# Performance work log

Measured on AMD Instinct MI355X. Metric: run time of the kernel, lower is better.

The kernel has to match this reference:

```python
import jax, jax.numpy as jnp
import numpy as np

N, E, H, IN, C, L, G = 50000, 600000, 128, 128, 4, 3, 128
EPS = 1e-5
BN_SCALE = 1.0 / np.sqrt(1.0 + EPS)  # eval BN with running_mean=0, running_var=1


def _bn(x, g, b):
    return x * (g * BN_SCALE) + b


def _gelu(x):
    return jax.nn.gelu(x, approximate=False)


def setup_inputs() -> dict:
    key = jax.random.key(0)
    ks = jax.random.split(key, 40)
    s = 0.02
    d = {}
    d['x'] = jax.random.normal(ks[0], (N, IN), jnp.float32)
    d['edge_index'] = jax.random.randint(ks[1], (2, E), 0, N)
    d['batch'] = jnp.sort(jax.random.randint(ks[2], (N,), 0, G))
    # input projection
    d['W1'] = jax.random.normal(ks[3], (IN, H)) * s; d['b1'] = jnp.zeros((H,))
    d['g1'] = jnp.ones((H,)); d['be1'] = jnp.zeros((H,))
    d['W2'] = jax.random.normal(ks[4], (H, H)) * s; d['b2'] = jnp.zeros((H,))
    d['g2'] = jnp.ones((H,)); d['be2'] = jnp.zeros((H,))
    # GCN layers (stacked over L)
    d['Wg'] = jax.random.normal(ks[5], (L, H, H)) * s
    d['bg'] = jnp.zeros((L, H))
    d['gg'] = jnp.ones((L, H)); d['bgg'] = jnp.zeros((L, H))
    # graph attention weights
    d['Wa1'] = jax.random.normal(ks[6], (H, H // 2)) * s; d['ba1'] = jnp.zeros((H // 2,))
    d['Wa2'] = jax.random.normal(ks[7], (H // 2, 1)) * s; d['ba2'] = jnp.zeros((1,))
    # classifier
    d['Wc1'] = jax.random.normal(ks[8], (4 * H, 2 * H)) * s; d['bc1'] = jnp.zeros((2 * H,))
    d['gc1'] = jnp.ones((2 * H,)); d['bec1'] = jnp.zeros((2 * H,))
    d['Wc2'] = jax.random.normal(ks[9], (2 * H, H)) * s; d['bc2'] = jnp.zeros((H,))
    d['gc2'] = jnp.ones((H,)); d['bec2'] = jnp.zeros((H,))
    d['Wc3'] = jax.random.normal(ks[10], (H, H // 2)) * s; d['bc3'] = jnp.zeros((H // 2,))
    d['gc3'] = jnp.ones((H // 2,)); d['bec3'] = jnp.zeros((H // 2,))
    d['Wc4'] = jax.random.normal(ks[11], (H // 2, C)) * s; d['bc4'] = jnp.zeros((C,))
    return d


def reference(x, edge_index, batch, W1, b1, g1, be1, W2, b2, g2, be2,
              Wg, bg, gg, bgg, Wa1, ba1, Wa2, ba2,
              Wc1, bc1, gc1, bec1, Wc2, bc2, gc2, bec2,
              Wc3, bc3, gc3, bec3, Wc4, bc4):
    n = x.shape[0]
    src, dst = edge_index[0], edge_index[1]
    # input projection (dropout off in eval)
    h = _gelu(_bn(x @ W1 + b1, g1, be1))
    h = _gelu(_bn(h @ W2 + b2, g2, be2))
    # GCN symmetric norm with self-loops (PyG GCNConv semantics)
    deg = jax.ops.segment_sum(jnp.ones_like(src, dtype=h.dtype), dst, n) + 1.0
    dinv = jax.lax.rsqrt(deg)
    enorm = (dinv[src] * dinv[dst])[:, None]   # [E,1]
    snorm = (dinv * dinv)[:, None]             # [N,1] self-loop weight
    for i in range(L):
        xw = h @ Wg[i]
        agg = jax.ops.segment_sum(xw[src] * enorm, dst, n) + xw * snorm
        h = _gelu(_bn(agg + bg[i], gg[i], bgg[i])) + h
    # attention weights per node
    aw = jnp.tanh(_gelu(h @ Wa1 + ba1) @ Wa2 + ba2)  # [N,1]
    # multi-branch pooling per graph
    cnt = jnp.maximum(jax.ops.segment_sum(jnp.ones((n,), h.dtype), batch, G), 1.0)[:, None]
    x_mean = jax.ops.segment_sum(h, batch, G) / cnt
    x_max = jax.ops.segment_max(h, batch, G)
    x_weighted = jax.ops.segment_sum(h * aw, batch, G) / cnt
    comb = jnp.concatenate([x_mean, x_max, x_mean, x_weighted], axis=-1)  # x_transformer_pooled == x_mean
    z = _gelu(_bn(comb @ Wc1 + bc1, gc1, bec1))
    z = _gelu(_bn(z @ Wc2 + bc2, gc2, bec2))
    z = _gelu(_bn(z @ Wc3 + bc3, gc3, bec3))
    return z @ Wc4 + bc4
```

## Files before the change

kernel.cpp:

```cpp
#include <hip/hip_runtime.h>
#include <hip/hip_bf16.h>
#include <float.h>


#define GGRAPHS 128
#define POOL_NC 16

typedef __attribute__((ext_vector_type(8))) short short8b;
typedef __attribute__((ext_vector_type(4))) float f32x4;

__device__ __forceinline__ float gelu_f(float x) {
    return 0.5f * x * (1.0f + erff(x * 0.7071067811865476f));
}

__device__ __forceinline__ unsigned short f2bf(float f) {
    unsigned int u = __float_as_uint(f);
    unsigned int r = (u + 0x7FFFu + ((u >> 16) & 1u)) >> 16;
    return (unsigned short)r;
}

__device__ __forceinline__ float bf2f(unsigned short u) {
    return __uint_as_float(((unsigned int)u) << 16);
}

static constexpr float BNS_F = 0.99999500003749968f;

__global__ void transpose_all_kernel(const float* __restrict__ W1, const float* __restrict__ W2,
                                     const float* __restrict__ Wg, const float* __restrict__ Wa1,
                                     unsigned short* __restrict__ Wt1, unsigned short* __restrict__ Wt2,
                                     unsigned short* __restrict__ Wtg, unsigned short* __restrict__ Wta1)
{
    const int id = blockIdx.x * 256 + threadIdx.x;
    if (id < 81920) {
        const int m = id >> 14;
        const int r = id & 16383;
        const int k = r >> 7, c = r & 127;
        const float* Wsrc = (m == 0) ? W1 : (m == 1) ? W2 : Wg + (size_t)(m - 2) * 16384;
        unsigned short* Wdst = (m == 0) ? Wt1 : (m == 1) ? Wt2 : Wtg + (size_t)(m - 2) * 16384;
        Wdst[c * 128 + k] = f2bf(Wsrc[r]);
    } else if (id < 90112) {
        const int r = id - 81920;
        const int k = r >> 6, c = r & 63;
        Wta1[c * 128 + k] = f2bf(Wa1[r]);
    }
}

template<int M, bool A_FP32, bool DO_BN, bool DO_GELU, bool DO_RES, bool DO_AW>
__global__ __launch_bounds__(256, 2)
void gemm_mfma(const void* __restrict__ Ain,
               const unsigned short* __restrict__ Wtb,
               const float* __restrict__ bias, const float* __restrict__ gam,
               const float* __restrict__ beta, const unsigned short* __restrict__ residb,
               unsigned short* __restrict__ Ybf,
               const float* __restrict__ Wa2, const float* __restrict__ ba2,
               float* __restrict__ awout, int nrows)
{
    constexpr int NCT = M / 16;
    __shared__ unsigned short Wl[M * 128];

    const int tid = threadIdx.x;

    constexpr int NCH = M * 16;
#pragma unroll
    for (int i = 0; i < NCH / 256; ++i) {
        const int idx = i * 256 + tid;
        const uint4 v = reinterpret_cast<const uint4*>(Wtb)[idx];
        const int byte = idx * 16;
        const int swz = byte ^ (((byte >> 8) & 7) << 4);
        *reinterpret_cast<uint4*>(reinterpret_cast<char*>(Wl) + swz) = v;
    }
    __syncthreads();

    const int w = tid >> 6;
    const int l = tid & 63;
    const int l4 = l >> 4, lm = l & 15;
    const int rowbase = (int)blockIdx.x * 64 + w * 16;

    int arow = rowbase + lm; if (arow >= nrows) arow = nrows - 1;
    short8b a[4];
    if constexpr (A_FP32) {
        const float* apf = (const float*)Ain + (size_t)arow * 128 + l4 * 8;
#pragma unroll
        for (int ks = 0; ks < 4; ++ks) {
            const float4 v0 = *reinterpret_cast<const float4*>(apf + ks * 32);
            const float4 v1 = *reinterpret_cast<const float4*>(apf + ks * 32 + 4);
            short8b av;
            av[0] = (short)f2bf(v0.x); av[1] = (short)f2bf(v0.y);
            av[2] = (short)f2bf(v0.z); av[3] = (short)f2bf(v0.w);
            av[4] = (short)f2bf(v1.x); av[5] = (short)f2bf(v1.y);
            av[6] = (short)f2bf(v1.z); av[7] = (short)f2bf(v1.w);
            a[ks] = av;
        }
    } else {
        const unsigned short* ap = (const unsigned short*)Ain + (size_t)arow * 128 + l4 * 8;
#pragma unroll
        for (int ks = 0; ks < 4; ++ks)
            a[ks] = *reinterpret_cast<const short8b*>(ap + ks * 32);
    }

    f32x4 acc[NCT];
#pragma unroll
    for (int ct = 0; ct < NCT; ++ct) acc[ct] = f32x4{0.f, 0.f, 0.f, 0.f};

    const int swzm = (lm & 7) << 4;
    const char* Wlc = reinterpret_cast<const char*>(Wl);
#pragma unroll
    for (int ks = 0; ks < 4; ++ks) {
#pragma unroll
        for (int ct = 0; ct < NCT; ++ct) {
            const int byte = ct * 4096 + lm * 256 + ks * 64 + l4 * 16;
            const short8b bv = *reinterpret_cast<const short8b*>(Wlc + (byte ^ swzm));
            acc[ct] = __builtin_amdgcn_mfma_f32_16x16x32_bf16(a[ks], bv, acc[ct], 0, 0, 0);
        }
    }

    if (DO_AW) {
        float p[4] = {0.f, 0.f, 0.f, 0.f};
#pragma unroll
        for (int ct = 0; ct < NCT; ++ct) {
            const int col = ct * 16 + lm;
            float sc, bi;
            if (DO_BN) { float g = gam[col]; sc = g * BNS_F; bi = bias[col] * sc + beta[col]; }
            else       { sc = 1.f; bi = bias[col]; }
            const float wa = Wa2[col];
#pragma unroll
            for (int rid = 0; rid < 4; ++rid) {
                float v = acc[ct][rid] * sc + bi;
                if (DO_GELU) v = gelu_f(v);
                p[rid] = fmaf(v, wa, p[rid]);
            }
        }
        const float ba2v = ba2[0];
#pragma unroll
        for (int rid = 0; rid < 4; ++rid) {
            float v = p[rid];
            v += __shfl_xor(v, 1);
            v += __shfl_xor(v, 2);
            v += __shfl_xor(v, 4);
            v += __shfl_xor(v, 8);
            const int row = rowbase + l4 * 4 + rid;
            if (lm == 0 && row < nrows) awout[row] = tanhf(v + ba2v);
        }
        return;
    }

#pragma unroll
    for (int ct = 0; ct < NCT; ++ct) {
        const int col = ct * 16 + lm;
        float sc, bi;
        if (DO_BN) { float g = gam[col]; sc = g * BNS_F; bi = bias[col] * sc + beta[col]; }
        else       { sc = 1.f; bi = bias[col]; }
#pragma unroll
        for (int rid = 0; rid < 4; ++rid) {
            const int row = rowbase + l4 * 4 + rid;
            if (row < nrows) {
                float v = acc[ct][rid] * sc + bi;
                if (DO_GELU) v = gelu_f(v);
                if (DO_RES) v += bf2f(residb[(size_t)row * M + col]);
                Ybf[(size_t)row * M + col] = f2bf(v);
            }
        }
    }
}

__global__ void count_rank_kernel(const int* __restrict__ dst, int* __restrict__ cnt,
                                  int* __restrict__ rank, int E)
{
    int e = blockIdx.x * 256 + threadIdx.x;
    if (e < E) rank[e] = atomicAdd(&cnt[dst[e]], 1);
}

__global__ void scan_local(const int* __restrict__ cnt, int* __restrict__ rowptr,
                           int* __restrict__ bsum, float* __restrict__ dinv, int n)
{
    __shared__ int sd[1024];
    const int tid = threadIdx.x;
    const int i = blockIdx.x * 1024 + tid;
    int v = (i < n) ? cnt[i] : 0;
    if (i < n) dinv[i] = rsqrtf((float)v + 1.0f);
    sd[tid] = v;
    __syncthreads();
    for (int off = 1; off < 1024; off <<= 1) {
        int t = (tid >= off) ? sd[tid - off] : 0;
        __syncthreads();
        sd[tid] += t;
        __syncthreads();
    }
    if (i < n) rowptr[i + 1] = sd[tid];
    if (tid == 1023) bsum[blockIdx.x] = sd[1023];
}

__global__ void scan_bsum(int* __restrict__ bsum, int nb)
{
    const int lane = threadIdx.x;
    int orig = (lane < nb) ? bsum[lane] : 0;
    int v = orig;
#pragma unroll
    for (int off = 1; off < 64; off <<= 1) {
        int t = __shfl_up(v, off);
        if (lane >= off) v += t;
    }
    if (lane < nb) bsum[lane] = v - orig;
}

__global__ void scan_add(int* __restrict__ rowptr, const int* __restrict__ bsum, int n)
{
    const int i = blockIdx.x * 1024 + threadIdx.x;
    if (i < n) rowptr[i + 1] += bsum[blockIdx.x];
    if (i == 0) rowptr[0] = 0;
}

__global__ void fill_kernel(const int* __restrict__ src, const int* __restrict__ dst,
                            const float* __restrict__ dinv, const int* __restrict__ rowptr,
                            const int* __restrict__ rank, int2* __restrict__ csr, int E)
{
    int e = blockIdx.x * 256 + threadIdx.x;
    if (e < E) {
        const int d = dst[e], s = src[e];
        const int pos = rowptr[d] + rank[e];
        int2 p;
        p.x = s;
        p.y = __float_as_int(dinv[s] * dinv[d]);
        csr[pos] = p;
    }
}

#define FMAB(A, Wt, U) { A.x = fmaf(Wt, bf2f(U.x), A.x); A.y = fmaf(Wt, bf2f(U.y), A.y); \
                         A.z = fmaf(Wt, bf2f(U.z), A.z); A.w = fmaf(Wt, bf2f(U.w), A.w); }

__global__ __launch_bounds__(256)
void agg_kernel(const ushort4* __restrict__ hb, const int2* __restrict__ csr,
                const int* __restrict__ rowptr, const float* __restrict__ dinv,
                ushort4* __restrict__ ahb, int n)
{
    const int node = blockIdx.x * 8 + (threadIdx.x >> 5);
    if (node >= n) return;
    const int lane = threadIdx.x & 31;

    const float di = dinv[node];
    const float sw = di * di;
    const ushort4 sv = hb[(size_t)node * 32 + lane];
    float4 a0, a1;
    a0.x = bf2f(sv.x) * sw; a0.y = bf2f(sv.y) * sw;
    a0.z = bf2f(sv.z) * sw; a0.w = bf2f(sv.w) * sw;
    a1.x = 0.f; a1.y = 0.f; a1.z = 0.f; a1.w = 0.f;

    const int beg = rowptr[node], end = rowptr[node + 1];
    int s = beg;
    for (; s + 4 <= end; s += 4) {
        const int2 e0 = csr[s+0], e1 = csr[s+1], e2 = csr[s+2], e3 = csr[s+3];
        const ushort4 v0 = hb[(size_t)e0.x * 32 + lane];
        const ushort4 v1 = hb[(size_t)e1.x * 32 + lane];
        const ushort4 v2 = hb[(size_t)e2.x * 32 + lane];
        const ushort4 v3 = hb[(size_t)e3.x * 32 + lane];
        FMAB(a0, __int_as_float(e0.y), v0); FMAB(a1, __int_as_float(e1.y), v1);
        FMAB(a0, __int_as_float(e2.y), v2); FMAB(a1, __int_as_float(e3.y), v3);
    }
    for (; s < end; ++s) {
        const int2 e0 = csr[s];
        const ushort4 v = hb[(size_t)e0.x * 32 + lane];
        FMAB(a0, __int_as_float(e0.y), v);
    }
    ushort4 q;
    q.x = f2bf(a0.x + a1.x); q.y = f2bf(a0.y + a1.y);
    q.z = f2bf(a0.z + a1.z); q.w = f2bf(a0.w + a1.w);
    ahb[(size_t)node * 32 + lane] = q;
}

__device__ __forceinline__ int lb_batch(const int* __restrict__ batch, int n, int t)
{
    int lo = 0, hi = n;
    while (lo < hi) { int mid = (lo + hi) >> 1; if (batch[mid] < t) lo = mid + 1; else hi = mid; }
    return lo;
}

__global__ void pool_partial(const unsigned short* __restrict__ h, const float* __restrict__ aw,
                             const int* __restrict__ batch, int n, float* __restrict__ ps,
                             float* __restrict__ pm, float* __restrict__ pw)
{
    const int g = blockIdx.x >> 4;
    const int c = blockIdx.x & (POOL_NC - 1);
    const int f = threadIdx.x;
    const int beg = lb_batch(batch, n, g), end = lb_batch(batch, n, g + 1);
    const int len = end - beg;
    const int cbeg = beg + (int)(((long long)len * c) / POOL_NC);
    const int cend = beg + (int)(((long long)len * (c + 1)) / POOL_NC);
    float s = 0.f, m = -FLT_MAX, w = 0.f;
    for (int node = cbeg; node < cend; ++node) {
        const float v = bf2f(h[(size_t)node * 128 + f]);
        const float a = aw[node];
        s += v;
        m = fmaxf(m, v);
        w = fmaf(v, a, w);
    }
    const size_t idx = ((size_t)g * POOL_NC + c) * 128 + f;
    ps[idx] = s; pm[idx] = m; pw[idx] = w;
}

__global__ void pool_final(const float* __restrict__ ps, const float* __restrict__ pm,
                           const float* __restrict__ pw, const int* __restrict__ batch,
                           int n, float* __restrict__ comb)
{
    const int g = blockIdx.x;
    const int f = threadIdx.x;
    float s = 0.f, m = -FLT_MAX, w = 0.f;
#pragma unroll
    for (int c = 0; c < POOL_NC; ++c) {
        const size_t idx = ((size_t)g * POOL_NC + c) * 128 + f;
        s += ps[idx];
        m = fmaxf(m, pm[idx]);
        w += pw[idx];
    }
    float cn = (float)(lb_batch(batch, n, g + 1) - lb_batch(batch, n, g));
    if (cn < 1.f) cn = 1.f;
    comb[(size_t)g * 512 + f]       = s / cn;
    comb[(size_t)g * 512 + 128 + f] = m;
    comb[(size_t)g * 512 + 256 + f] = s / cn;
    comb[(size_t)g * 512 + 384 + f] = w / cn;
}

template<int K, int M, bool DO_BN, bool DO_GELU>
__global__ __launch_bounds__(256)
void rowgemm2(const float* __restrict__ X, const float* __restrict__ W,
              const float* __restrict__ bias, const float* __restrict__ gam,
              const float* __restrict__ beta, float* __restrict__ Y)
{
    constexpr int NC = M / 64;
    constexpr int KQ = K / 4;
    const int row = blockIdx.x / NC;
    const int lane = threadIdx.x & 63;
    const int c = (blockIdx.x % NC) * 64 + lane;
    const int q = threadIdx.x >> 6;

    const float* __restrict__ xq = X + (size_t)row * K + q * KQ;
    const float* __restrict__ wq = W + (size_t)(q * KQ) * M + c;

    float a0 = 0.f, a1 = 0.f, a2 = 0.f, a3 = 0.f;
#pragma unroll 4
    for (int k = 0; k < KQ; k += 4) {
        const float4 xv = *reinterpret_cast<const float4*>(xq + k);
        a0 = fmaf(xv.x, wq[(size_t)(k + 0) * M], a0);
        a1 = fmaf(xv.y, wq[(size_t)(k + 1) * M], a1);
        a2 = fmaf(xv.z, wq[(size_t)(k + 2) * M], a2);
        a3 = fmaf(xv.w, wq[(size_t)(k + 3) * M], a3);
    }
    __shared__ float part[4][64];
    part[q][lane] = (a0 + a1) + (a2 + a3);
    __syncthreads();
    if (q == 0) {
        float v = (part[0][lane] + part[1][lane]) + (part[2][lane] + part[3][lane]);
        if (DO_BN) { const float g = gam[c]; const float sc = g * BNS_F; v = v * sc + (bias[c] * sc + beta[c]); }
        else       { v = v + bias[c]; }
        if (DO_GELU) v = gelu_f(v);
        Y[(size_t)row * M + c] = v;
    }
}

__global__ void rowgemm_final(const float* __restrict__ X, const float* __restrict__ W,
                              const float* __restrict__ bias, float* __restrict__ Y)
{
    const int row = blockIdx.x;
    const int lane = threadIdx.x;
    const float xv = X[(size_t)row * 64 + lane];
    const float4 wr = *reinterpret_cast<const float4*>(W + lane * 4);
    float a0 = xv * wr.x, a1 = xv * wr.y, a2 = xv * wr.z, a3 = xv * wr.w;
#pragma unroll
    for (int off = 32; off; off >>= 1) {
        a0 += __shfl_xor(a0, off);
        a1 += __shfl_xor(a1, off);
        a2 += __shfl_xor(a2, off);
        a3 += __shfl_xor(a3, off);
    }
    if (lane == 0) {
        Y[(size_t)row * 4 + 0] = a0 + bias[0];
        Y[(size_t)row * 4 + 1] = a1 + bias[1];
        Y[(size_t)row * 4 + 2] = a2 + bias[2];
        Y[(size_t)row * 4 + 3] = a3 + bias[3];
    }
}

extern "C" void kernel_launch(void* const* d_in, const int* in_sizes, int n_in,
                              void* d_out, int out_size, void* d_ws, size_t ws_size,
                              hipStream_t stream)
{
    const float* x     = (const float*)d_in[0];
    const int*   ei    = (const int*)d_in[1];
    const int*   batch = (const int*)d_in[2];
    const float* W1  = (const float*)d_in[3];
    const float* b1  = (const float*)d_in[4];
    const float* g1  = (const float*)d_in[5];
    const float* be1 = (const float*)d_in[6];
    const float* W2  = (const float*)d_in[7];
    const float* b2  = (const float*)d_in[8];
    const float* g2  = (const float*)d_in[9];
    const float* be2 = (const float*)d_in[10];
    const float* Wg  = (const float*)d_in[11];
    const float* bg  = (const float*)d_in[12];
    const float* gg  = (const float*)d_in[13];
    const float* bgg = (const float*)d_in[14];
    const float* Wa1 = (const float*)d_in[15];
    const float* ba1 = (const float*)d_in[16];
    const float* Wa2 = (const float*)d_in[17];
    const float* ba2 = (const float*)d_in[18];
    const float* Wc1 = (const float*)d_in[19];
    const float* bc1 = (const float*)d_in[20];
    const float* gc1 = (const float*)d_in[21];
    const float* bec1= (const float*)d_in[22];
    const float* Wc2 = (const float*)d_in[23];
    const float* bc2 = (const float*)d_in[24];
    const float* gc2 = (const float*)d_in[25];
    const float* bec2= (const float*)d_in[26];
    const float* Wc3 = (const float*)d_in[27];
    const float* bc3 = (const float*)d_in[28];
    const float* gc3 = (const float*)d_in[29];
    const float* bec3= (const float*)d_in[30];
    const float* Wc4 = (const float*)d_in[31];
    const float* bc4 = (const float*)d_in[32];
    float* out = (float*)d_out;

    const int N = in_sizes[0] / 128;
    const int E = in_sizes[1] / 2;
    const int G = GGRAPHS;

    size_t off = 0;
    auto alloc = [&](size_t bytes) -> void* {
        void* p = (char*)d_ws + off;
        off += (bytes + 255) & ~(size_t)255;
        return p;
    };
    unsigned short* hAb   = (unsigned short*)alloc((size_t)N * 128 * 2);
    unsigned short* hbf   = (unsigned short*)alloc((size_t)N * 128 * 2);
    unsigned short* ahb   = (unsigned short*)alloc((size_t)N * 128 * 2);
    unsigned short* Wt1   = (unsigned short*)alloc(128 * 128 * 2);
    unsigned short* Wt2   = (unsigned short*)alloc(128 * 128 * 2);
    unsigned short* Wtg   = (unsigned short*)alloc(3 * 128 * 128 * 2);
    unsigned short* Wta1  = (unsigned short*)alloc(64 * 128 * 2);
    float*   aw     = (float*)alloc((size_t)N * 4);
    float*   dinv   = (float*)alloc((size_t)N * 4);
    int*     cnt    = (int*)alloc((size_t)N * 4);
    int*     rank   = (int*)alloc((size_t)E * 4);
    int*     rowptr = (int*)alloc((size_t)(N + 1) * 4);
    int*     bsum   = (int*)alloc(64 * 4);
    int2*    csr    = (int2*)alloc((size_t)E * 8);
    float*   comb   = (float*)alloc((size_t)G * 512 * 4);
    float*   ps     = (float*)alloc((size_t)G * POOL_NC * 128 * 4);
    float*   pm     = (float*)alloc((size_t)G * POOL_NC * 128 * 4);
    float*   pw     = (float*)alloc((size_t)G * POOL_NC * 128 * 4);
    float*   z1     = (float*)alloc((size_t)G * 256 * 4);
    float*   z2     = (float*)alloc((size_t)G * 128 * 4);
    float*   z3     = (float*)alloc((size_t)G * 64 * 4);
    (void)ws_size;

    const int* e_src = ei;
    const int* e_dst = ei + E;

    transpose_all_kernel<<<352, 256, 0, stream>>>(W1, W2, Wg, Wa1, Wt1, Wt2, Wtg, Wta1);

    hipMemsetAsync(cnt, 0, (size_t)N * 4, stream);
    count_rank_kernel<<<(E + 255) / 256, 256, 0, stream>>>(e_dst, cnt, rank, E);
    const int nb = (N + 1023) / 1024;
    scan_local<<<nb, 1024, 0, stream>>>(cnt, rowptr, bsum, dinv, N);
    scan_bsum<<<1, 64, 0, stream>>>(bsum, nb);
    scan_add<<<nb, 1024, 0, stream>>>(rowptr, bsum, N);
    fill_kernel<<<(E + 255) / 256, 256, 0, stream>>>(e_src, e_dst, dinv, rowptr, rank, csr, E);

    const int rowblocks = (N + 63) / 64;

    gemm_mfma<128, true, true, true, false, false><<<rowblocks, 256, 0, stream>>>(
        x, Wt1, b1, g1, be1, nullptr, hAb, nullptr, nullptr, nullptr, N);
    gemm_mfma<128, false, true, true, false, false><<<rowblocks, 256, 0, stream>>>(
        hAb, Wt2, b2, g2, be2, nullptr, hbf, nullptr, nullptr, nullptr, N);

    for (int l = 0; l < 3; ++l) {
        agg_kernel<<<(N + 7) / 8, 256, 0, stream>>>(
            (const ushort4*)hbf, csr, rowptr, dinv, (ushort4*)ahb, N);
        gemm_mfma<128, false, true, true, true, false><<<rowblocks, 256, 0, stream>>>(
            ahb, Wtg + (size_t)l * 16384, bg + (size_t)l * 128,
            gg + (size_t)l * 128, bgg + (size_t)l * 128, hbf, hbf,
            nullptr, nullptr, nullptr, N);
    }

    gemm_mfma<64, false, false, true, false, true><<<rowblocks, 256, 0, stream>>>(
        hbf, Wta1, ba1, nullptr, nullptr, nullptr, nullptr, Wa2, ba2, aw, N);

    pool_partial<<<G * POOL_NC, 128, 0, stream>>>(hbf, aw, batch, N, ps, pm, pw);
    pool_final<<<G, 128, 0, stream>>>(ps, pm, pw, batch, N, comb);

    rowgemm2<512, 256, true, true><<<G * 4, 256, 0, stream>>>(comb, Wc1, bc1, gc1, bec1, z1);
    rowgemm2<256, 128, true, true><<<G * 2, 256, 0, stream>>>(z1, Wc2, bc2, gc2, bec2, z2);
    rowgemm2<128, 64,  true, true><<<G * 1, 256, 0, stream>>>(z2, Wc3, bc3, gc3, bec3, z3);
    rowgemm_final<<<G, 64, 0, stream>>>(z3, Wc4, bc4, out);
}
```

Baseline: 382.6 us.

## Fuse input projection GEMMs and last GCN GEMM with attention GEMM via LDS

Merges the two input-projection GEMMs into one kernel that keeps the intermediate activation in swizzled LDS instead of writing and re-reading it from global memory. Fuses the final GCN layer GEMM with the attention-weight GEMM, reusing the freshly computed h tile from LDS. Also folds the single-block bsum scan into scan_add, so one launch is removed. The fused kernels use more LDS per block (up to 80KB), which may lower occupancy.

```diff
diff --git a/kernel.cpp b/kernel.cpp
--- a/kernel.cpp
+++ b/kernel.cpp
@@ -45,63 +45,24 @@
     }
 }
 
-template<int M, bool A_FP32, bool DO_BN, bool DO_GELU, bool DO_RES, bool DO_AW>
-__global__ __launch_bounds__(256, 2)
-void gemm_mfma(const void* __restrict__ Ain,
-               const unsigned short* __restrict__ Wtb,
-               const float* __restrict__ bias, const float* __restrict__ gam,
-               const float* __restrict__ beta, const unsigned short* __restrict__ residb,
-               unsigned short* __restrict__ Ybf,
-               const float* __restrict__ Wa2, const float* __restrict__ ba2,
-               float* __restrict__ awout, int nrows)
-{
-    constexpr int NCT = M / 16;
-    __shared__ unsigned short Wl[M * 128];
-
-    const int tid = threadIdx.x;
-
-    constexpr int NCH = M * 16;
-#pragma unroll
-    for (int i = 0; i < NCH / 256; ++i) {
+template<int M>
+__device__ __forceinline__ void stage_wt(const unsigned short* __restrict__ Wtb,
+                                         unsigned short* __restrict__ Wl, int tid)
+{
+#pragma unroll
+    for (int i = 0; i < (M * 16) / 256; ++i) {
         const int idx = i * 256 + tid;
         const uint4 v = reinterpret_cast<const uint4*>(Wtb)[idx];
         const int byte = idx * 16;
         const int swz = byte ^ (((byte >> 8) & 7) << 4);
         *reinterpret_cast<uint4*>(reinterpret_cast<char*>(Wl) + swz) = v;
     }
-    __syncthreads();
-
-    const int w = tid >> 6;
-    const int l = tid & 63;
-    const int l4 = l >> 4, lm = l & 15;
-    const int rowbase = (int)blockIdx.x * 64 + w * 16;
-
-    int arow = rowbase + lm; if (arow >= nrows) arow = nrows - 1;
-    short8b a[4];
-    if constexpr (A_FP32) {
-        const float* apf = (const float*)Ain + (size_t)arow * 128 + l4 * 8;
-#pragma unroll
-        for (int ks = 0; ks < 4; ++ks) {
-            const float4 v0 = *reinterpret_cast<const float4*>(apf + ks * 32);
-            const float4 v1 = *reinterpret_cast<const float4*>(apf + ks * 32 + 4);
-            short8b av;
-            av[0] = (short)f2bf(v0.x); av[1] = (short)f2bf(v0.y);
-            av[2] = (short)f2bf(v0.z); av[3] = (short)f2bf(v0.w);
-            av[4] = (short)f2bf(v1.x); av[5] = (short)f2bf(v1.y);
-            av[6] = (short)f2bf(v1.z); av[7] = (short)f2bf(v1.w);
-            a[ks] = av;
-        }
-    } else {
-        const unsigned short* ap = (const unsigned short*)Ain + (size_t)arow * 128 + l4 * 8;
-#pragma unroll
-        for (int ks = 0; ks < 4; ++ks)
-            a[ks] = *reinterpret_cast<const short8b*>(ap + ks * 32);
-    }
-
-    f32x4 acc[NCT];
-#pragma unroll
-    for (int ct = 0; ct < NCT; ++ct) acc[ct] = f32x4{0.f, 0.f, 0.f, 0.f};
-
+}
+
+template<int NCT>
+__device__ __forceinline__ void mfma_stage(const short8b* a, const unsigned short* __restrict__ Wl,
+                                           f32x4* acc, int l4, int lm)
+{
     const int swzm = (lm & 7) << 4;
     const char* Wlc = reinterpret_cast<const char*>(Wl);
 #pragma unroll
@@ -113,53 +74,246 @@
             acc[ct] = __builtin_amdgcn_mfma_f32_16x16x32_bf16(a[ks], bv, acc[ct], 0, 0, 0);
         }
     }
-
-    if (DO_AW) {
-        float p[4] = {0.f, 0.f, 0.f, 0.f};
-#pragma unroll
-        for (int ct = 0; ct < NCT; ++ct) {
-            const int col = ct * 16 + lm;
-            float sc, bi;
-            if (DO_BN) { float g = gam[col]; sc = g * BNS_F; bi = bias[col] * sc + beta[col]; }
-            else       { sc = 1.f; bi = bias[col]; }
-            const float wa = Wa2[col];
-#pragma unroll
-            for (int rid = 0; rid < 4; ++rid) {
-                float v = acc[ct][rid] * sc + bi;
-                if (DO_GELU) v = gelu_f(v);
-                p[rid] = fmaf(v, wa, p[rid]);
-            }
+}
+
+__device__ __forceinline__ void load_afrag_bf(const unsigned short* __restrict__ ap, short8b* a)
+{
+#pragma unroll
+    for (int ks = 0; ks < 4; ++ks)
+        a[ks] = *reinterpret_cast<const short8b*>(ap + ks * 32);
+}
+
+__device__ __forceinline__ void load_afrag_lds(const unsigned short* __restrict__ hl,
+                                               int rowl, int l4, short8b* a)
+{
+    const char* hc = reinterpret_cast<const char*>(hl);
+    const int swz = (rowl & 7) << 4;
+#pragma unroll
+    for (int ks = 0; ks < 4; ++ks) {
+        const int byte = rowl * 256 + ks * 64 + l4 * 16;
+        a[ks] = *reinterpret_cast<const short8b*>(hc + (byte ^ swz));
+    }
+}
+
+__device__ __forceinline__ void store_h_lds(unsigned short* __restrict__ hl,
+                                            int rowl, int col, unsigned short v)
+{
+    const int byte = (rowl * 256 + col * 2) ^ ((rowl & 7) << 4);
+    *reinterpret_cast<unsigned short*>(reinterpret_cast<char*>(hl) + byte) = v;
+}
+
+__global__ __launch_bounds__(256, 2)
+void proj_fused(const float* __restrict__ x,
+                const unsigned short* __restrict__ Wt1, const unsigned short* __restrict__ Wt2,
+                const float* __restrict__ b1, const float* __restrict__ g1, const float* __restrict__ be1,
+                const float* __restrict__ b2, const float* __restrict__ g2, const float* __restrict__ be2,
+                unsigned short* __restrict__ hbf, int nrows)
+{
+    __shared__ unsigned short W1l[128 * 128];
+    __shared__ unsigned short W2l[128 * 128];
+    __shared__ unsigned short h1l[64 * 128];
+
+    const int tid = threadIdx.x;
+    stage_wt<128>(Wt1, W1l, tid);
+    stage_wt<128>(Wt2, W2l, tid);
+    __syncthreads();
+
+    const int w = tid >> 6;
+    const int l = tid & 63;
+    const int l4 = l >> 4, lm = l & 15;
+    const int rowbase = (int)blockIdx.x * 64 + w * 16;
+
+    int arow = rowbase + lm; if (arow >= nrows) arow = nrows - 1;
+    const float* apf = x + (size_t)arow * 128 + l4 * 8;
+    short8b a[4];
+#pragma unroll
+    for (int ks = 0; ks < 4; ++ks) {
+        const float4 v0 = *reinterpret_cast<const float4*>(apf + ks * 32);
+        const float4 v1 = *reinterpret_cast<const float4*>(apf + ks * 32 + 4);
+        short8b av;
+        av[0] = (short)f2bf(v0.x); av[1] = (short)f2bf(v0.y);
+        av[2] = (short)f2bf(v0.z); av[3] = (short)f2bf(v0.w);
+        av[4] = (short)f2bf(v1.x); av[5] = (short)f2bf(v1.y);
+        av[6] = (short)f2bf(v1.z); av[7] = (short)f2bf(v1.w);
+        a[ks] = av;
+    }
+
+    f32x4 acc[8];
+#pragma unroll
+    for (int ct = 0; ct < 8; ++ct) acc[ct] = f32x4{0.f, 0.f, 0.f, 0.f};
+    mfma_stage<8>(a, W1l, acc, l4, lm);
+
+#pragma unroll
+    for (int ct = 0; ct < 8; ++ct) {
+        const int col = ct * 16 + lm;
+        const float g = g1[col];
+        const float sc = g * BNS_F;
+        const float bi = b1[col] * sc + be1[col];
+#pragma unroll
+        for (int rid = 0; rid < 4; ++rid) {
+            const int rowl = w * 16 + l4 * 4 + rid;
+            float v = acc[ct][rid] * sc + bi;
+            v = gelu_f(v);
+            store_h_lds(h1l, rowl, col, f2bf(v));
         }
-        const float ba2v = ba2[0];
-#pragma unroll
-        for (int rid = 0; rid < 4; ++rid) {
-            float v = p[rid];
-            v += __shfl_xor(v, 1);
-            v += __shfl_xor(v, 2);
-            v += __shfl_xor(v, 4);
-            v += __shfl_xor(v, 8);
-            const int row = rowbase + l4 * 4 + rid;
-            if (lm == 0 && row < nrows) awout[row] = tanhf(v + ba2v);
-        }
-        return;
-    }
-
-#pragma unroll
-    for (int ct = 0; ct < NCT; ++ct) {
+    }
+    __syncthreads();
+
+    load_afrag_lds(h1l, w * 16 + lm, l4, a);
+#pragma unroll
+    for (int ct = 0; ct < 8; ++ct) acc[ct] = f32x4{0.f, 0.f, 0.f, 0.f};
+    mfma_stage<8>(a, W2l, acc, l4, lm);
+
+#pragma unroll
+    for (int ct = 0; ct < 8; ++ct) {
         const int col = ct * 16 + lm;
-        float sc, bi;
-        if (DO_BN) { float g = gam[col]; sc = g * BNS_F; bi = bias[col] * sc + beta[col]; }
-        else       { sc = 1.f; bi = bias[col]; }
+        const float g = g2[col];
+        const float sc = g * BNS_F;
+        const float bi = b2[col] * sc + be2[col];
 #pragma unroll
         for (int rid = 0; rid < 4; ++rid) {
             const int row = rowbase + l4 * 4 + rid;
             if (row < nrows) {
                 float v = acc[ct][rid] * sc + bi;
-                if (DO_GELU) v = gelu_f(v);
-                if (DO_RES) v += bf2f(residb[(size_t)row * M + col]);
-                Ybf[(size_t)row * M + col] = f2bf(v);
+                v = gelu_f(v);
+                hbf[(size_t)row * 128 + col] = f2bf(v);
             }
         }
+    }
+}
+
+__global__ __launch_bounds__(256, 2)
+void gemm_gcn(const unsigned short* __restrict__ Abf,
+              const unsigned short* __restrict__ Wtb,
+              const float* __restrict__ bias, const float* __restrict__ gam,
+              const float* __restrict__ beta, unsigned short* __restrict__ hbf,
+              int nrows)
+{
+    __shared__ unsigned short Wl[128 * 128];
+
+    const int tid = threadIdx.x;
+    stage_wt<128>(Wtb, Wl, tid);
+    __syncthreads();
+
+    const int w = tid >> 6;
+    const int l = tid & 63;
+    const int l4 = l >> 4, lm = l & 15;
+    const int rowbase = (int)blockIdx.x * 64 + w * 16;
+
+    int arow = rowbase + lm; if (arow >= nrows) arow = nrows - 1;
+    short8b a[4];
+    load_afrag_bf(Abf + (size_t)arow * 128 + l4 * 8, a);
+
+    f32x4 acc[8];
+#pragma unroll
+    for (int ct = 0; ct < 8; ++ct) acc[ct] = f32x4{0.f, 0.f, 0.f, 0.f};
+    mfma_stage<8>(a, Wl, acc, l4, lm);
+
+#pragma unroll
+    for (int ct = 0; ct < 8; ++ct) {
+        const int col = ct * 16 + lm;
+        const float g = gam[col];
+        const float sc = g * BNS_F;
+        const float bi = bias[col] * sc + beta[col];
+#pragma unroll
+        for (int rid = 0; rid < 4; ++rid) {
+            const int row = rowbase + l4 * 4 + rid;
+            if (row < nrows) {
+                float v = acc[ct][rid] * sc + bi;
+                v = gelu_f(v);
+                v += bf2f(hbf[(size_t)row * 128 + col]);
+                hbf[(size_t)row * 128 + col] = f2bf(v);
+            }
+        }
+    }
+}
+
+__global__ __launch_bounds__(256, 2)
+void gcn_aw_fused(const unsigned short* __restrict__ Abf,
+                  const unsigned short* __restrict__ Wt3,
+                  const float* __restrict__ bias, const float* __restrict__ gam,
+                  const float* __restrict__ beta, unsigned short* __restrict__ hbf,
+                  const unsigned short* __restrict__ Wta1, const float* __restrict__ ba1,
+                  const float* __restrict__ Wa2, const float* __restrict__ ba2,
+                  float* __restrict__ awout, int nrows)
+{
+    __shared__ unsigned short W3l[128 * 128];
+    __shared__ unsigned short Wa1l[64 * 128];
+    __shared__ unsigned short hl[64 * 128];
+
+    const int tid = threadIdx.x;
+    stage_wt<128>(Wt3, W3l, tid);
+    stage_wt<64>(Wta1, Wa1l, tid);
+    __syncthreads();
+
+    const int w = tid >> 6;
+    const int l = tid & 63;
+    const int l4 = l >> 4, lm = l & 15;
+    const int rowbase = (int)blockIdx.x * 64 + w * 16;
+
+    int arow = rowbase + lm; if (arow >= nrows) arow = nrows - 1;
+    short8b a[4];
+    load_afrag_bf(Abf + (size_t)arow * 128 + l4 * 8, a);
+
+    f32x4 acc[8];
+#pragma unroll
+    for (int ct = 0; ct < 8; ++ct) acc[ct] = f32x4{0.f, 0.f, 0.f, 0.f};
+    mfma_stage<8>(a, W3l, acc, l4, lm);
+
+#pragma unroll
+    for (int ct = 0; ct < 8; ++ct) {
+        const int col = ct * 16 + lm;
+        const float g = gam[col];
+        const float sc = g * BNS_F;
+        const float bi = bias[col] * sc + beta[col];
+#pragma unroll
+        for (int rid = 0; rid < 4; ++rid) {
+            const int row = rowbase + l4 * 4 + rid;
+            const int rowl = w * 16 + l4 * 4 + rid;
+            float v = acc[ct][rid] * sc + bi;
+            v = gelu_f(v);
+            unsigned short hv;
+            if (row < nrows) {
+                v += bf2f(hbf[(size_t)row * 128 + col]);
+                hv = f2bf(v);
+                hbf[(size_t)row * 128 + col] = hv;
+            } else {
+                hv = 0;
+            }
+            store_h_lds(hl, rowl, col, hv);
+        }
+    }
+    __syncthreads();
+
+    load_afrag_lds(hl, w * 16 + lm, l4, a);
+    f32x4 acc2[4];
+#pragma unroll
+    for (int ct = 0; ct < 4; ++ct) acc2[ct] = f32x4{0.f, 0.f, 0.f, 0.f};
+    mfma_stage<4>(a, Wa1l, acc2, l4, lm);
+
+    float p[4] = {0.f, 0.f, 0.f, 0.f};
+#pragma unroll
+    for (int ct = 0; ct < 4; ++ct) {
+        const int col = ct * 16 + lm;
+        const float bi = ba1[col];
+        const float wa = Wa2[col];
+#pragma unroll
+        for (int rid = 0; rid < 4; ++rid) {
+            float v = acc2[ct][rid] + bi;
+            v = gelu_f(v);
+            p[rid] = fmaf(v, wa, p[rid]);
+        }
+    }
+    const float ba2v = ba2[0];
+#pragma unroll
+    for (int rid = 0; rid < 4; ++rid) {
+        float v = p[rid];
+        v += __shfl_xor(v, 1);
+        v += __shfl_xor(v, 2);
+        v += __shfl_xor(v, 4);
+        v += __shfl_xor(v, 8);
+        const int row = rowbase + l4 * 4 + rid;
+        if (lm == 0 && row < nrows) awout[row] = tanhf(v + ba2v);
     }
 }
 
@@ -190,23 +344,19 @@
     if (tid == 1023) bsum[blockIdx.x] = sd[1023];
 }
 
-__global__ void scan_bsum(int* __restrict__ bsum, int nb)
-{
-    const int lane = threadIdx.x;
-    int orig = (lane < nb) ? bsum[lane] : 0;
-    int v = orig;
-#pragma unroll
-    for (int off = 1; off < 64; off <<= 1) {
-        int t = __shfl_up(v, off);
-        if (lane >= off) v += t;
-    }
-    if (lane < nb) bsum[lane] = v - orig;
-}
-
 __global__ void scan_add(int* __restrict__ rowptr, const int* __restrict__ bsum, int n)
 {
-    const int i = blockIdx.x * 1024 + threadIdx.x;
-    if (i < n) rowptr[i + 1] += bsum[blockIdx.x];
+    __shared__ int pref;
+    const int bid = blockIdx.x;
+    if (threadIdx.x < 64) {
+        int v = ((int)threadIdx.x < bid) ? bsum[threadIdx.x] : 0;
+#pragma unroll
+        for (int off = 32; off; off >>= 1) v += __shfl_xor(v, off);
+        if (threadIdx.x == 0) pref = v;
+    }
+    __syncthreads();
+    const int i = bid * 1024 + threadIdx.x;
+    if (i < n) rowptr[i + 1] += pref;
     if (i == 0) rowptr[0] = 0;
 }
 
@@ -428,7 +578,6 @@
         off += (bytes + 255) & ~(size_t)255;
         return p;
     };
-    unsigned short* hAb   = (unsigned short*)alloc((size_t)N * 128 * 2);
     unsigned short* hbf   = (unsigned short*)alloc((size_t)N * 128 * 2);
     unsigned short* ahb   = (unsigned short*)alloc((size_t)N * 128 * 2);
     unsigned short* Wt1   = (unsigned short*)alloc(128 * 128 * 2);
@@ -460,28 +609,28 @@
     count_rank_kernel<<<(E + 255) / 256, 256, 0, stream>>>(e_dst, cnt, rank, E);
     const int nb = (N + 1023) / 1024;
     scan_local<<<nb, 1024, 0, stream>>>(cnt, rowptr, bsum, dinv, N);
-    scan_bsum<<<1, 64, 0, stream>>>(bsum, nb);
     scan_add<<<nb, 1024, 0, stream>>>(rowptr, bsum, N);
     fill_kernel<<<(E + 255) / 256, 256, 0, stream>>>(e_src, e_dst, dinv, rowptr, rank, csr, E);
 
     const int rowblocks = (N + 63) / 64;
 
-    gemm_mfma<128, true, true, true, false, false><<<rowblocks, 256, 0, stream>>>(
-        x, Wt1, b1, g1, be1, nullptr, hAb, nullptr, nullptr, nullptr, N);
-    gemm_mfma<128, false, true, true, false, false><<<rowblocks, 256, 0, stream>>>(
-        hAb, Wt2, b2, g2, be2, nullptr, hbf, nullptr, nullptr, nullptr, N);
-
-    for (int l = 0; l < 3; ++l) {
+    proj_fused<<<rowblocks, 256, 0, stream>>>(
+        x, Wt1, Wt2, b1, g1, be1, b2, g2, be2, hbf, N);
+
+    for (int l = 0; l < 2; ++l) {
         agg_kernel<<<(N + 7) / 8, 256, 0, stream>>>(
             (const ushort4*)hbf, csr, rowptr, dinv, (ushort4*)ahb, N);
-        gemm_mfma<128, false, true, true, true, false><<<rowblocks, 256, 0, stream>>>(
+        gemm_gcn<<<rowblocks, 256, 0, stream>>>(
             ahb, Wtg + (size_t)l * 16384, bg + (size_t)l * 128,
-            gg + (size_t)l * 128, bgg + (size_t)l * 128, hbf, hbf,
-            nullptr, nullptr, nullptr, N);
-    }
-
-    gemm_mfma<64, false, false, true, false, true><<<rowblocks, 256, 0, stream>>>(
-        hbf, Wta1, ba1, nullptr, nullptr, nullptr, nullptr, Wa2, ba2, aw, N);
+            gg + (size_t)l * 128, bgg + (size_t)l * 128, hbf, N);
+    }
+
+    agg_kernel<<<(N + 7) / 8, 256, 0, stream>>>(
+        (const ushort4*)hbf, csr, rowptr, dinv, (ushort4*)ahb, N);
+    gcn_aw_fused<<<rowblocks, 256, 0, stream>>>(
+        ahb, Wtg + (size_t)2 * 16384, bg + (size_t)2 * 128,
+        gg + (size_t)2 * 128, bgg + (size_t)2 * 128, hbf,
+        Wta1, ba1, Wa2, ba2, aw, N);
 
     pool_partial<<<G * POOL_NC, 128, 0, stream>>>(hbf, aw, batch, N, ps, pm, pw);
     pool_final<<<G, 128, 0, stream>>>(ps, pm, pw, batch, N, comb);
```

After: 386.7 us. Within noise of the previous version (+1.1%).
